# Kernel optimization log

Measured on AMD Instinct MI355X. Metric: run time of the kernel, lower is better.

## Reference

```python
import jax, jax.numpy as jnp
import numpy as np

N = 6607   # gene_num
H = 64     # hidden_channels
T = 3      # number of edge types
E = 1_000_000  # edges per type


def setup_inputs() -> dict:
    key = jax.random.key(0)
    ks = jax.random.split(key, 9)
    emb = jax.random.normal(ks[0], (N, H), dtype=jnp.float32) * 0.1
    edge_index = jax.random.randint(ks[1], (T, 2, E), 0, N)
    W1l = jax.random.normal(ks[2], (T, H, H), dtype=jnp.float32) * 0.1
    b1 = jnp.zeros((T, H), dtype=jnp.float32)
    W1r = jax.random.normal(ks[3], (T, H, H), dtype=jnp.float32) * 0.1
    W2l = jax.random.normal(ks[4], (T, H, H), dtype=jnp.float32) * 0.1
    b2 = jnp.zeros((T, H), dtype=jnp.float32)
    W2r = jax.random.normal(ks[5], (T, H, H), dtype=jnp.float32) * 0.1
    Wrec = jax.random.normal(ks[6], (T, N, H), dtype=jnp.float32) * 0.1
    brec = jnp.zeros((T, N), dtype=jnp.float32)
    return dict(emb=emb, edge_index=edge_index, W1l=W1l, b1=b1, W1r=W1r,
                W2l=W2l, b2=b2, W2r=W2r, Wrec=Wrec, brec=brec)


def _sage(x, src, dst, Wl, bl, Wr):
    # PyG SAGEConv (mean aggr, normalize=False, project=False):
    #   out = lin_l(mean_{j in N(i)} x_j) + lin_r(x_i); bias only on lin_l.
    agg = jax.ops.segment_sum(x[src], dst, num_segments=N)        # [N, H]
    deg = jax.ops.segment_sum(jnp.ones((src.shape[0],), x.dtype), dst, num_segments=N)
    agg = agg / jnp.maximum(deg, 1.0)[:, None]                    # mean, isolated nodes -> 0
    return agg @ Wl.T + bl + x @ Wr.T


def reference(emb, edge_index, W1l, b1, W1r, W2l, b2, W2r, Wrec, brec):
    x_init = emb  # embedding(arange(N)) is the full table

    def per_type(ei, w1l, bb1, w1r, w2l, bb2, w2r, wrec, bbrec):
        src, dst = ei[0], ei[1]
        h1 = jax.nn.relu(_sage(x_init, src, dst, w1l, bb1, w1r))  # [N, H]
        h2 = jax.nn.relu(_sage(h1, src, dst, w2l, bb2, w2r))      # [N, H]
        recon = h2 @ wrec.T + bbrec                               # [N, N]
        return h2, recon

    embeddings, reconstructions = jax.vmap(per_type)(
        edge_index, W1l, b1, W1r, W2l, b2, W2r, Wrec, brec)
    return embeddings, reconstructions, x_init
```

## Files before the change

### kernel.cpp

```cpp
#include <hip/hip_runtime.h>
#include <hip/hip_bf16.h>

#define NN 6607
#define HH 64
#define TT 3
#define EE 1000000
#define KSH 50

typedef __attribute__((ext_vector_type(8))) short bf16x8;
typedef __attribute__((ext_vector_type(4))) short short4v;
typedef __attribute__((ext_vector_type(4))) float f32x4;
typedef __attribute__((ext_vector_type(2))) float f32x2;
typedef __attribute__((ext_vector_type(4))) int i32x4;

#define LGKM_BARRIER() do { \
    __builtin_amdgcn_sched_barrier(0); \
    asm volatile("s_waitcnt lgkmcnt(0)" ::: "memory"); \
    __builtin_amdgcn_s_barrier(); \
    __builtin_amdgcn_sched_barrier(0); \
} while (0)


__global__ void prep_hist_kernel(const float* __restrict__ wrec, short* __restrict__ wrecb,
                                 const float* __restrict__ emb, float* __restrict__ o_xinit,
                                 const int* __restrict__ ei, unsigned short* __restrict__ H) {
    if (blockIdx.x < KSH * TT) {
        int k = blockIdx.x % KSH, t = blockIdx.x / KSH;
        __shared__ int h[NN];
        for (int i = threadIdx.x; i < NN; i += 1024) h[i] = 0;
        __syncthreads();
        const int2* d2 = (const int2*)(ei + t * 2 * EE + EE + k * (EE / KSH));
        for (int i = threadIdx.x; i < (EE / KSH) / 2; i += 1024) {
            int2 p = d2[i];
            atomicAdd(&h[p.x], 1);
            atomicAdd(&h[p.y], 1);
        }
        __syncthreads();
        unsigned short* Ht = H + (size_t)(t * KSH + k) * NN;
        for (int i = threadIdx.x; i < NN; i += 1024) Ht[i] = (unsigned short)h[i];
    } else {
        int i = (blockIdx.x - KSH * TT) * 1024 + threadIdx.x;
        if (i < 105712) ((f32x4*)o_xinit)[i] = ((const f32x4*)emb)[i];
        if (i < 317136) {
            f32x4 v = ((const f32x4*)wrec)[i];
            short4v s;
            s[0] = (short)__bfloat16_as_ushort(__float2bfloat16(v[0]));
            s[1] = (short)__bfloat16_as_ushort(__float2bfloat16(v[1]));
            s[2] = (short)__bfloat16_as_ushort(__float2bfloat16(v[2]));
            s[3] = (short)__bfloat16_as_ushort(__float2bfloat16(v[3]));
            ((short4v*)wrecb)[i] = s;
        }
    }
}

__global__ void off2a_kernel(unsigned short* __restrict__ H, int* __restrict__ degI) {
    int t = blockIdx.y;
    int i = blockIdx.x * 256 + threadIdx.x;
    if (i >= NN) return;
    int run = 0;
    #pragma unroll
    for (int k = 0; k < KSH; ++k) {
        unsigned short* p = H + (size_t)(t * KSH + k) * NN + i;
        int v = *p; *p = (unsigned short)run; run += v;
    }
    degI[t * NN + i] = run;
}

__global__ void off2b_kernel(const int* __restrict__ degI, int* __restrict__ basep) {
    int t = blockIdx.x;
    int lane = threadIdx.x;
    const int* d = degI + t * NN;
    int* bp = basep + t * NN;
    int carry = 0;
    for (int b0 = 0; b0 < NN; b0 += 64) {
        int i = b0 + lane;
        int v = (i < NN) ? d[i] : 0;
        int s = v;
        #pragma unroll
        for (int off = 1; off < 64; off <<= 1) {
            int u = __shfl_up(s, off, 64);
            if (lane >= off) s += u;
        }
        if (i < NN) bp[i] = carry + s - v;
        carry += __shfl(s, 63, 64);
    }
}

__global__ void fill3_kernel(const int* __restrict__ ei, const unsigned short* __restrict__ H,
                             const int* __restrict__ basep, int* __restrict__ csr) {
    int k = blockIdx.x, t = blockIdx.y;
    __shared__ int cur[NN];
    const unsigned short* Ht = H + (size_t)(t * KSH + k) * NN;
    const int* bp = basep + t * NN;
    for (int i = threadIdx.x; i < NN; i += 1024) cur[i] = bp[i] + (int)Ht[i];
    __syncthreads();
    const int2* s2 = (const int2*)(ei + t * 2 * EE + k * (EE / KSH));
    const int2* d2 = (const int2*)(ei + t * 2 * EE + EE + k * (EE / KSH));
    int* cs = csr + t * EE;
    for (int i = threadIdx.x; i < (EE / KSH) / 2; i += 1024) {
        int2 d = d2[i], s = s2[i];
        int p0 = atomicAdd(&cur[d.x], 1);
        cs[p0] = s.x;
        int p1 = atomicAdd(&cur[d.y], 1);
        cs[p1] = s.y;
    }
}


template <int LAYER>
__global__ void __launch_bounds__(512) sage_kernel(
        const float* __restrict__ x_all,
        const int* __restrict__ basep, const int* __restrict__ degI,
        const int* __restrict__ csr,
        const float* __restrict__ W_l, const float* __restrict__ b_l,
        const float* __restrict__ W_r, float* __restrict__ y) {
    int t = blockIdx.y;
    __shared__ float wl[64][68];
    __shared__ float wr[64][68];
    __shared__ float mean_s[8][64];
    __shared__ float xi_s[8][64];
    const f32x4* Wl4 = (const f32x4*)(W_l + t * 4096);
    const f32x4* Wr4 = (const f32x4*)(W_r + t * 4096);
    for (int cc = threadIdx.x; cc < 1024; cc += 512) {
        int h = cc >> 4, k = (cc & 15) << 2;
        *(f32x4*)&wl[h][k] = Wl4[cc];
        *(f32x4*)&wr[h][k] = Wr4[cc];
    }
    __syncthreads();

    int lane = threadIdx.x & 63;
    int widx = threadIdx.x >> 6;
    int i = blockIdx.x * 8 + widx;
    if (i >= NN) return;

    const float* x = x_all + (LAYER == 2 ? (size_t)t * NN * HH : 0);
    const f32x2* x2 = (const f32x2*)x;
    int rp0 = basep[t * NN + i];
    int d = degI[t * NN + i];
    int rp1 = rp0 + d;
    const int* cs = csr + t * EE;

    int h2 = lane >> 5;
    int c = lane & 31;

    f32x2 ac0 = {0.f, 0.f}, ac1 = {0.f, 0.f}, ac2 = {0.f, 0.f}, ac3 = {0.f, 0.f};
    int e = rp0;
    if ((e & 1) && e < rp1) {
        if (h2 == 0) ac0 += x2[(size_t)cs[e] * 32 + c];
        ++e;
    }
    for (; e + 8 <= rp1; e += 8) {
        const int2* q = (const int2*)(cs + e) + 2 * h2;
        int2 p0 = q[0], p1 = q[1];
        ac0 += x2[(size_t)p0.x * 32 + c];
        ac1 += x2[(size_t)p0.y * 32 + c];
        ac2 += x2[(size_t)p1.x * 32 + c];
        ac3 += x2[(size_t)p1.y * 32 + c];
    }
    f32x2 accT = (ac0 + ac1) + (ac2 + ac3);
    if (h2 == 0) {
        for (; e < rp1; ++e) accT += x2[(size_t)cs[e] * 32 + c];
    }
    accT[0] += __shfl_xor(accT[0], 32, 64);
    accT[1] += __shfl_xor(accT[1], 32, 64);

    float inv = 1.f / (float)(d > 1 ? d : 1);
    f32x2 mean2 = accT * inv;
    f32x2 xi2 = x2[(size_t)i * 32 + c];

    if (h2 == 0) {
        *(f32x2*)&mean_s[widx][2 * c] = mean2;
        *(f32x2*)&xi_s[widx][2 * c] = xi2;
    }

    float out = b_l[t * 64 + lane];
    #pragma unroll 4
    for (int k0 = 0; k0 < 64; k0 += 4) {
        f32x4 m4 = *(const f32x4*)&mean_s[widx][k0];
        f32x4 x4 = *(const f32x4*)&xi_s[widx][k0];
        f32x4 l4 = *(const f32x4*)&wl[lane][k0];
        f32x4 r4 = *(const f32x4*)&wr[lane][k0];
        out += m4[0] * l4[0] + m4[1] * l4[1] + m4[2] * l4[2] + m4[3] * l4[3];
        out += x4[0] * r4[0] + x4[1] * r4[1] + x4[2] * r4[2] + x4[3] * r4[3];
    }
    out = fmaxf(out, 0.f);
    y[(size_t)t * NN * HH + i * 64 + lane] = out;
}


__global__ void __launch_bounds__(256) recon_kernel(
        const float* __restrict__ h2f, const short* __restrict__ wrecb,
        const float* __restrict__ brec, float* __restrict__ out) {
    constexpr int NI = (NN + 15) / 16;
    constexpr int NG = 7;
    __shared__ float buf[16][260];

    int bid = blockIdx.x;
    int t = bid / (NI * NG);
    int rem = bid % (NI * NG);
    int jg = rem / NI;
    int it = rem % NI;
    int i0 = it * 16;
    int colbase = jg * 1024;
    int nch = (NN - colbase + 255) / 256;
    if (nch > 4) nch = 4;

    int tid = threadIdx.x;
    int lane = tid & 63;
    int w = tid >> 6;
    int r = lane & 15;
    int kb = (lane >> 4) * 8;
    int rbase = (lane >> 4) * 4;

    const float* A = h2f + (size_t)t * NN * HH;
    const short* B = wrecb + (size_t)t * NN * HH;
    const float* br = brec + t * NN;
    size_t obase = (size_t)t * NN * NN;

    f32x4 af0 = *(const f32x4*)(A + (size_t)(i0 + r) * 64 + kb);
    f32x4 af1 = *(const f32x4*)(A + (size_t)(i0 + r) * 64 + kb + 4);
    f32x4 af2 = *(const f32x4*)(A + (size_t)(i0 + r) * 64 + kb + 32);
    f32x4 af3 = *(const f32x4*)(A + (size_t)(i0 + r) * 64 + kb + 36);
    bf16x8 a0, a1;
    #pragma unroll
    for (int q = 0; q < 4; ++q) {
        a0[q]     = (short)__bfloat16_as_ushort(__float2bfloat16(af0[q]));
        a0[q + 4] = (short)__bfloat16_as_ushort(__float2bfloat16(af1[q]));
        a1[q]     = (short)__bfloat16_as_ushort(__float2bfloat16(af2[q]));
        a1[q + 4] = (short)__bfloat16_as_ushort(__float2bfloat16(af3[q]));
    }

    int scol = lane << 2;

    bf16x8 Breg[8];
    float biasreg[4];

    auto loadB = [&](int chunk) {
        int jbase = colbase + chunk * 256 + w * 64;
        #pragma unroll
        for (int jt = 0; jt < 4; ++jt) {
            int j0 = jbase + jt * 16;
            Breg[2 * jt]     = *(const bf16x8*)(B + (size_t)(j0 + r) * 64 + kb);
            Breg[2 * jt + 1] = *(const bf16x8*)(B + (size_t)(j0 + r) * 64 + kb + 32);
            int col = j0 + r;
            col = col < NN ? col : NN - 1;
            biasreg[jt] = br[col];
        }
    };

    auto mfma_phase = [&]() {
        #pragma unroll
        for (int jt = 0; jt < 4; ++jt) {
            float bb = biasreg[jt];
            f32x4 acc = {bb, bb, bb, bb};
            acc = __builtin_amdgcn_mfma_f32_16x16x32_bf16(a0, Breg[2 * jt], acc, 0, 0, 0);
            acc = __builtin_amdgcn_mfma_f32_16x16x32_bf16(a1, Breg[2 * jt + 1], acc, 0, 0, 0);
            int jloc = w * 64 + jt * 16 + r;
            #pragma unroll
            for (int q = 0; q < 4; ++q) buf[rbase + q][jloc] = acc[q];
        }
    };

    auto store_phase = [&](int chunk) {
        int colg = colbase + chunk * 256 + scol;
        if (colg >= NN) return;
        bool full4 = (colg + 4 <= NN);
        #pragma unroll
        for (int p = 0; p < 4; ++p) {
            int rloc = p * 4 + w;
            int row = i0 + rloc;
            if (row >= NN) continue;
            f32x4 v = *(const f32x4*)&buf[rloc][scol];
            float* pp = out + obase + (size_t)row * NN + colg;
            if (full4) {
                __builtin_nontemporal_store(v, (f32x4*)pp);
            } else {
                __builtin_nontemporal_store(v[0], pp);
                if (colg + 1 < NN) __builtin_nontemporal_store(v[1], pp + 1);
                if (colg + 2 < NN) __builtin_nontemporal_store(v[2], pp + 2);
            }
        }
    };

    loadB(0);
    mfma_phase();
    LGKM_BARRIER();
    for (int cch = 1; cch < nch; ++cch) {
        loadB(cch);
        store_phase(cch - 1);
        LGKM_BARRIER();
        mfma_phase();
        LGKM_BARRIER();
    }
    store_phase(nch - 1);
}


extern "C" void kernel_launch(void* const* d_in, const int* in_sizes, int n_in,
                              void* d_out, int out_size, void* d_ws, size_t ws_size,
                              hipStream_t stream) {
    const float* emb  = (const float*)d_in[0];
    const int*   ei   = (const int*)d_in[1];
    const float* W1l  = (const float*)d_in[2];
    const float* b1   = (const float*)d_in[3];
    const float* W1r  = (const float*)d_in[4];
    const float* W2l  = (const float*)d_in[5];
    const float* b2   = (const float*)d_in[6];
    const float* W2r  = (const float*)d_in[7];
    const float* Wrec = (const float*)d_in[8];
    const float* brec = (const float*)d_in[9];

    char* ws = (char*)d_ws;
    int*            degI  = (int*)(ws + 0);
    int*            basep = (int*)(ws + 79296);
    int*            csr   = (int*)(ws + 158592);
    unsigned short* H     = (unsigned short*)(ws + 12158592);
    float*          h1    = (float*)(ws + 14140800);
    short*          wrecb = (short*)(ws + 19214976);

    float* o_emb   = (float*)d_out;
    float* o_recon = o_emb + (size_t)TT * NN * HH;
    float* o_xinit = o_recon + (size_t)TT * NN * NN;

    int phgrid = KSH * TT + (317136 + 1023) / 1024;
    prep_hist_kernel<<<phgrid, 1024, 0, stream>>>(Wrec, wrecb, emb, o_xinit, ei, H);
    dim3 o2grid((NN + 255) / 256, TT);
    off2a_kernel<<<o2grid, 256, 0, stream>>>(H, degI);
    off2b_kernel<<<TT, 64, 0, stream>>>(degI, basep);
    dim3 fgrid(KSH, TT);
    fill3_kernel<<<fgrid, 1024, 0, stream>>>(ei, H, basep, csr);

    dim3 sgrid((NN + 7) / 8, TT);
    sage_kernel<1><<<sgrid, 512, 0, stream>>>(emb, basep, degI, csr, W1l, b1, W1r, h1);
    sage_kernel<2><<<sgrid, 512, 0, stream>>>(h1, basep, degI, csr, W2l, b2, W2r, o_emb);

    constexpr int NI = (NN + 15) / 16;
    constexpr int NG = 7;
    int rblocks = NI * NG * TT;
    recon_kernel<<<rblocks, 256, 0, stream>>>(o_emb, wrecb, brec, o_recon);
}
```

Before: 411.1 us.

## Restructure recon kernel to compute full 16x1024 tile in LDS before storing

The reconstruction kernel now uses 512 threads. Each of its 8 waves computes 128 output columns, covering the whole 16x1024 tile in one pass into a larger LDS buffer, followed by a single barrier and a store phase. This replaces the old 4-chunk loop that overlapped B loads, MFMA and stores through repeated LGKM barriers. The bias is now added during the store instead of seeding the accumulator. The aim is fewer barriers and more parallel waves issuing loads and stores, at the cost of about 66KB of LDS per block (which can limit occupancy) and no explicit compute/store overlap.

```diff
diff --git a/kernel.cpp b/kernel.cpp
--- a/kernel.cpp
+++ b/kernel.cpp
@@ -12,13 +12,6 @@
 typedef __attribute__((ext_vector_type(4))) float f32x4;
 typedef __attribute__((ext_vector_type(2))) float f32x2;
 typedef __attribute__((ext_vector_type(4))) int i32x4;
-
-#define LGKM_BARRIER() do { \
-    __builtin_amdgcn_sched_barrier(0); \
-    asm volatile("s_waitcnt lgkmcnt(0)" ::: "memory"); \
-    __builtin_amdgcn_s_barrier(); \
-    __builtin_amdgcn_sched_barrier(0); \
-} while (0)
 
 
 __global__ void prep_hist_kernel(const float* __restrict__ wrec, short* __restrict__ wrecb,
@@ -188,12 +181,12 @@
 }
 
 
-__global__ void __launch_bounds__(256) recon_kernel(
+__global__ void __launch_bounds__(512) recon_kernel(
         const float* __restrict__ h2f, const short* __restrict__ wrecb,
         const float* __restrict__ brec, float* __restrict__ out) {
     constexpr int NI = (NN + 15) / 16;
     constexpr int NG = 7;
-    __shared__ float buf[16][260];
+    __shared__ float buf[16][1036];
 
     int bid = blockIdx.x;
     int t = bid / (NI * NG);
@@ -202,8 +195,6 @@
     int it = rem % NI;
     int i0 = it * 16;
     int colbase = jg * 1024;
-    int nch = (NN - colbase + 255) / 256;
-    if (nch > 4) nch = 4;
 
     int tid = threadIdx.x;
     int lane = tid & 63;
@@ -230,69 +221,44 @@
         a1[q + 4] = (short)__bfloat16_as_ushort(__float2bfloat16(af3[q]));
     }
 
-    int scol = lane << 2;
-
-    bf16x8 Breg[8];
-    float biasreg[4];
-
-    auto loadB = [&](int chunk) {
-        int jbase = colbase + chunk * 256 + w * 64;
+    int jwbase = colbase + w * 128;
+    #pragma unroll
+    for (int jt = 0; jt < 8; ++jt) {
+        int j0 = jwbase + jt * 16;
+        bf16x8 b0 = *(const bf16x8*)(B + (size_t)(j0 + r) * 64 + kb);
+        bf16x8 b1 = *(const bf16x8*)(B + (size_t)(j0 + r) * 64 + kb + 32);
+        f32x4 acc = {0.f, 0.f, 0.f, 0.f};
+        acc = __builtin_amdgcn_mfma_f32_16x16x32_bf16(a0, b0, acc, 0, 0, 0);
+        acc = __builtin_amdgcn_mfma_f32_16x16x32_bf16(a1, b1, acc, 0, 0, 0);
+        int jloc = w * 128 + jt * 16 + r;
         #pragma unroll
-        for (int jt = 0; jt < 4; ++jt) {
-            int j0 = jbase + jt * 16;
-            Breg[2 * jt]     = *(const bf16x8*)(B + (size_t)(j0 + r) * 64 + kb);
-            Breg[2 * jt + 1] = *(const bf16x8*)(B + (size_t)(j0 + r) * 64 + kb + 32);
-            int col = j0 + r;
-            col = col < NN ? col : NN - 1;
-            biasreg[jt] = br[col];
-        }
-    };
-
-    auto mfma_phase = [&]() {
+        for (int q = 0; q < 4; ++q) buf[rbase + q][jloc] = acc[q];
+    }
+    __syncthreads();
+
+    #pragma unroll
+    for (int p = 0; p < 2; ++p) {
+        int rloc = 2 * w + p;
+        int row = i0 + rloc;
+        if (row >= NN) continue;
+        float* rowp = out + obase + (size_t)row * NN;
         #pragma unroll
-        for (int jt = 0; jt < 4; ++jt) {
-            float bb = biasreg[jt];
-            f32x4 acc = {bb, bb, bb, bb};
-            acc = __builtin_amdgcn_mfma_f32_16x16x32_bf16(a0, Breg[2 * jt], acc, 0, 0, 0);
-            acc = __builtin_amdgcn_mfma_f32_16x16x32_bf16(a1, Breg[2 * jt + 1], acc, 0, 0, 0);
-            int jloc = w * 64 + jt * 16 + r;
-            #pragma unroll
-            for (int q = 0; q < 4; ++q) buf[rbase + q][jloc] = acc[q];
-        }
-    };
-
-    auto store_phase = [&](int chunk) {
-        int colg = colbase + chunk * 256 + scol;
-        if (colg >= NN) return;
-        bool full4 = (colg + 4 <= NN);
-        #pragma unroll
-        for (int p = 0; p < 4; ++p) {
-            int rloc = p * 4 + w;
-            int row = i0 + rloc;
-            if (row >= NN) continue;
-            f32x4 v = *(const f32x4*)&buf[rloc][scol];
-            float* pp = out + obase + (size_t)row * NN + colg;
-            if (full4) {
-                __builtin_nontemporal_store(v, (f32x4*)pp);
+        for (int s = 0; s < 4; ++s) {
+            int cloc = s * 256 + (lane << 2);
+            int colg = colbase + cloc;
+            if (colg >= NN) continue;
+            f32x4 v = *(const f32x4*)&buf[rloc][cloc];
+            if (colg + 4 <= NN) {
+                f32x4 wv = {v[0] + br[colg], v[1] + br[colg + 1],
+                            v[2] + br[colg + 2], v[3] + br[colg + 3]};
+                __builtin_nontemporal_store(wv, (f32x4*)(rowp + colg));
             } else {
-                __builtin_nontemporal_store(v[0], pp);
-                if (colg + 1 < NN) __builtin_nontemporal_store(v[1], pp + 1);
-                if (colg + 2 < NN) __builtin_nontemporal_store(v[2], pp + 2);
+                __builtin_nontemporal_store(v[0] + br[colg], rowp + colg);
+                if (colg + 1 < NN) __builtin_nontemporal_store(v[1] + br[colg + 1], rowp + colg + 1);
+                if (colg + 2 < NN) __builtin_nontemporal_store(v[2] + br[colg + 2], rowp + colg + 2);
             }
         }
-    };
-
-    loadB(0);
-    mfma_phase();
-    LGKM_BARRIER();
-    for (int cch = 1; cch < nch; ++cch) {
-        loadB(cch);
-        store_phase(cch - 1);
-        LGKM_BARRIER();
-        mfma_phase();
-        LGKM_BARRIER();
-    }
-    store_phase(nch - 1);
+    }
 }
 
 
@@ -337,5 +303,5 @@
     constexpr int NI = (NN + 15) / 16;
     constexpr int NG = 7;
     int rblocks = NI * NG * TT;
-    recon_kernel<<<rblocks, 256, 0, stream>>>(o_emb, wrecb, brec, o_recon);
-}
+    recon_kernel<<<rblocks, 512, 0, stream>>>(o_emb, wrecb, brec, o_recon);
+}
```

Measured after the change: 451.8 us. 9.9% more time.

## Store CSR indices as uint16 and gather bf16 features in SAGE layers

Applied to the files above, without the earlier changes.

Node indices in the CSR are stored as 16-bit values, since N fits in 16 bits, which halves the index traffic. The embedding and layer-1 hidden features are converted to bf16, so each neighbour gather reads one 32-bit word per lane instead of a float2. Accumulation stays in fp32. The cost is bf16 rounding of the layer inputs and of the layer-1 output, which adds numerical error to h2 and to the reconstructions.

```diff
diff --git a/kernel.cpp b/kernel.cpp
--- a/kernel.cpp
+++ b/kernel.cpp
@@ -10,7 +10,6 @@
 typedef __attribute__((ext_vector_type(8))) short bf16x8;
 typedef __attribute__((ext_vector_type(4))) short short4v;
 typedef __attribute__((ext_vector_type(4))) float f32x4;
-typedef __attribute__((ext_vector_type(2))) float f32x2;
 typedef __attribute__((ext_vector_type(4))) int i32x4;
 
 #define LGKM_BARRIER() do { \
@@ -23,6 +22,7 @@
 
 __global__ void prep_hist_kernel(const float* __restrict__ wrec, short* __restrict__ wrecb,
                                  const float* __restrict__ emb, float* __restrict__ o_xinit,
+                                 short* __restrict__ embb,
                                  const int* __restrict__ ei, unsigned short* __restrict__ H) {
     if (blockIdx.x < KSH * TT) {
         int k = blockIdx.x % KSH, t = blockIdx.x / KSH;
@@ -40,7 +40,16 @@
         for (int i = threadIdx.x; i < NN; i += 1024) Ht[i] = (unsigned short)h[i];
     } else {
         int i = (blockIdx.x - KSH * TT) * 1024 + threadIdx.x;
-        if (i < 105712) ((f32x4*)o_xinit)[i] = ((const f32x4*)emb)[i];
+        if (i < 105712) {
+            f32x4 v = ((const f32x4*)emb)[i];
+            ((f32x4*)o_xinit)[i] = v;
+            short4v s;
+            s[0] = (short)__bfloat16_as_ushort(__float2bfloat16(v[0]));
+            s[1] = (short)__bfloat16_as_ushort(__float2bfloat16(v[1]));
+            s[2] = (short)__bfloat16_as_ushort(__float2bfloat16(v[2]));
+            s[3] = (short)__bfloat16_as_ushort(__float2bfloat16(v[3]));
+            ((short4v*)embb)[i] = s;
+        }
         if (i < 317136) {
             f32x4 v = ((const f32x4*)wrec)[i];
             short4v s;
@@ -87,7 +96,7 @@
 }
 
 __global__ void fill3_kernel(const int* __restrict__ ei, const unsigned short* __restrict__ H,
-                             const int* __restrict__ basep, int* __restrict__ csr) {
+                             const int* __restrict__ basep, unsigned short* __restrict__ csr) {
     int k = blockIdx.x, t = blockIdx.y;
     __shared__ int cur[NN];
     const unsigned short* Ht = H + (size_t)(t * KSH + k) * NN;
@@ -96,24 +105,25 @@
     __syncthreads();
     const int2* s2 = (const int2*)(ei + t * 2 * EE + k * (EE / KSH));
     const int2* d2 = (const int2*)(ei + t * 2 * EE + EE + k * (EE / KSH));
-    int* cs = csr + t * EE;
+    unsigned short* cs = csr + (size_t)t * EE;
     for (int i = threadIdx.x; i < (EE / KSH) / 2; i += 1024) {
         int2 d = d2[i], s = s2[i];
         int p0 = atomicAdd(&cur[d.x], 1);
-        cs[p0] = s.x;
+        cs[p0] = (unsigned short)s.x;
         int p1 = atomicAdd(&cur[d.y], 1);
-        cs[p1] = s.y;
+        cs[p1] = (unsigned short)s.y;
     }
 }
 
 
 template <int LAYER>
 __global__ void __launch_bounds__(512) sage_kernel(
-        const float* __restrict__ x_all,
+        const unsigned int* __restrict__ xb_all,
         const int* __restrict__ basep, const int* __restrict__ degI,
-        const int* __restrict__ csr,
+        const unsigned short* __restrict__ csr,
         const float* __restrict__ W_l, const float* __restrict__ b_l,
-        const float* __restrict__ W_r, float* __restrict__ y) {
+        const float* __restrict__ W_r,
+        float* __restrict__ yf, unsigned short* __restrict__ yb) {
     int t = blockIdx.y;
     __shared__ float wl[64][68];
     __shared__ float wr[64][68];
@@ -133,44 +143,57 @@
     int i = blockIdx.x * 8 + widx;
     if (i >= NN) return;
 
-    const float* x = x_all + (LAYER == 2 ? (size_t)t * NN * HH : 0);
-    const f32x2* x2 = (const f32x2*)x;
+    const unsigned int* xb = xb_all + (LAYER == 2 ? (size_t)t * NN * 32 : 0);
     int rp0 = basep[t * NN + i];
     int d = degI[t * NN + i];
     int rp1 = rp0 + d;
-    const int* cs = csr + t * EE;
+    const unsigned short* cs = csr + (size_t)t * EE;
 
     int h2 = lane >> 5;
     int c = lane & 31;
 
-    f32x2 ac0 = {0.f, 0.f}, ac1 = {0.f, 0.f}, ac2 = {0.f, 0.f}, ac3 = {0.f, 0.f};
+    float a0l = 0.f, a0h = 0.f, a1l = 0.f, a1h = 0.f;
+    float a2l = 0.f, a2h = 0.f, a3l = 0.f, a3h = 0.f;
     int e = rp0;
     if ((e & 1) && e < rp1) {
-        if (h2 == 0) ac0 += x2[(size_t)cs[e] * 32 + c];
+        if (h2 == 0) {
+            unsigned u = xb[(size_t)cs[e] * 32 + c];
+            a0l += __uint_as_float(u << 16);
+            a0h += __uint_as_float(u & 0xffff0000u);
+        }
         ++e;
     }
     for (; e + 8 <= rp1; e += 8) {
-        const int2* q = (const int2*)(cs + e) + 2 * h2;
-        int2 p0 = q[0], p1 = q[1];
-        ac0 += x2[(size_t)p0.x * 32 + c];
-        ac1 += x2[(size_t)p0.y * 32 + c];
-        ac2 += x2[(size_t)p1.x * 32 + c];
-        ac3 += x2[(size_t)p1.y * 32 + c];
-    }
-    f32x2 accT = (ac0 + ac1) + (ac2 + ac3);
+        const ushort2* q = (const ushort2*)(cs + e) + 2 * h2;
+        ushort2 p0 = q[0], p1 = q[1];
+        unsigned u0 = xb[(size_t)p0.x * 32 + c];
+        unsigned u1 = xb[(size_t)p0.y * 32 + c];
+        unsigned u2 = xb[(size_t)p1.x * 32 + c];
+        unsigned u3 = xb[(size_t)p1.y * 32 + c];
+        a0l += __uint_as_float(u0 << 16); a0h += __uint_as_float(u0 & 0xffff0000u);
+        a1l += __uint_as_float(u1 << 16); a1h += __uint_as_float(u1 & 0xffff0000u);
+        a2l += __uint_as_float(u2 << 16); a2h += __uint_as_float(u2 & 0xffff0000u);
+        a3l += __uint_as_float(u3 << 16); a3h += __uint_as_float(u3 & 0xffff0000u);
+    }
+    float al = (a0l + a1l) + (a2l + a3l);
+    float ah = (a0h + a1h) + (a2h + a3h);
     if (h2 == 0) {
-        for (; e < rp1; ++e) accT += x2[(size_t)cs[e] * 32 + c];
-    }
-    accT[0] += __shfl_xor(accT[0], 32, 64);
-    accT[1] += __shfl_xor(accT[1], 32, 64);
+        for (; e < rp1; ++e) {
+            unsigned u = xb[(size_t)cs[e] * 32 + c];
+            al += __uint_as_float(u << 16);
+            ah += __uint_as_float(u & 0xffff0000u);
+        }
+    }
+    al += __shfl_xor(al, 32, 64);
+    ah += __shfl_xor(ah, 32, 64);
 
     float inv = 1.f / (float)(d > 1 ? d : 1);
-    f32x2 mean2 = accT * inv;
-    f32x2 xi2 = x2[(size_t)i * 32 + c];
-
     if (h2 == 0) {
-        *(f32x2*)&mean_s[widx][2 * c] = mean2;
-        *(f32x2*)&xi_s[widx][2 * c] = xi2;
+        unsigned uxi = xb[(size_t)i * 32 + c];
+        mean_s[widx][2 * c]     = al * inv;
+        mean_s[widx][2 * c + 1] = ah * inv;
+        xi_s[widx][2 * c]     = __uint_as_float(uxi << 16);
+        xi_s[widx][2 * c + 1] = __uint_as_float(uxi & 0xffff0000u);
     }
 
     float out = b_l[t * 64 + lane];
@@ -184,7 +207,12 @@
         out += x4[0] * r4[0] + x4[1] * r4[1] + x4[2] * r4[2] + x4[3] * r4[3];
     }
     out = fmaxf(out, 0.f);
-    y[(size_t)t * NN * HH + i * 64 + lane] = out;
+    if (LAYER == 1) {
+        yb[(size_t)t * NN * HH + (size_t)i * 64 + lane] =
+            __bfloat16_as_ushort(__float2bfloat16(out));
+    } else {
+        yf[(size_t)t * NN * HH + (size_t)i * 64 + lane] = out;
+    }
 }
 
 
@@ -313,26 +341,29 @@
     char* ws = (char*)d_ws;
     int*            degI  = (int*)(ws + 0);
     int*            basep = (int*)(ws + 79296);
-    int*            csr   = (int*)(ws + 158592);
-    unsigned short* H     = (unsigned short*)(ws + 12158592);
-    float*          h1    = (float*)(ws + 14140800);
-    short*          wrecb = (short*)(ws + 19214976);
+    unsigned short* csrb  = (unsigned short*)(ws + 158592);
+    unsigned short* H     = (unsigned short*)(ws + 6158592);
+    unsigned short* h1b   = (unsigned short*)(ws + 8140800);
+    short*          embb  = (short*)(ws + 10677888);
+    short*          wrecb = (short*)(ws + 11523584);
 
     float* o_emb   = (float*)d_out;
     float* o_recon = o_emb + (size_t)TT * NN * HH;
     float* o_xinit = o_recon + (size_t)TT * NN * NN;
 
     int phgrid = KSH * TT + (317136 + 1023) / 1024;
-    prep_hist_kernel<<<phgrid, 1024, 0, stream>>>(Wrec, wrecb, emb, o_xinit, ei, H);
+    prep_hist_kernel<<<phgrid, 1024, 0, stream>>>(Wrec, wrecb, emb, o_xinit, embb, ei, H);
     dim3 o2grid((NN + 255) / 256, TT);
     off2a_kernel<<<o2grid, 256, 0, stream>>>(H, degI);
     off2b_kernel<<<TT, 64, 0, stream>>>(degI, basep);
     dim3 fgrid(KSH, TT);
-    fill3_kernel<<<fgrid, 1024, 0, stream>>>(ei, H, basep, csr);
+    fill3_kernel<<<fgrid, 1024, 0, stream>>>(ei, H, basep, csrb);
 
     dim3 sgrid((NN + 7) / 8, TT);
-    sage_kernel<1><<<sgrid, 512, 0, stream>>>(emb, basep, degI, csr, W1l, b1, W1r, h1);
-    sage_kernel<2><<<sgrid, 512, 0, stream>>>(h1, basep, degI, csr, W2l, b2, W2r, o_emb);
+    sage_kernel<1><<<sgrid, 512, 0, stream>>>((const unsigned int*)embb, basep, degI, csrb,
+                                              W1l, b1, W1r, nullptr, h1b);
+    sage_kernel<2><<<sgrid, 512, 0, stream>>>((const unsigned int*)h1b, basep, degI, csrb,
+                                              W2l, b2, W2r, o_emb, nullptr);
 
     constexpr int NI = (NN + 15) / 16;
     constexpr int NG = 7;
```

Result: faster. 359.6 us (-12.5%).
